# Kernel optimization log

Hardware: AMD Instinct MI355X
Metric: run time of the kernel (lower is better)

Reference implementation:

```python
import jax, jax.numpy as jnp
import numpy as np

N = 20000      # nodes
E = 640000     # edges (avg degree 32)
IN = 32        # input_dim
HID = 256      # hidden_dim
H = 8          # num_heads
Dh = HID // H  # head_dim = 32
TD = 32        # time_dim
L = 3          # num_layers
OUT = 2


def setup_inputs() -> dict:
    key = jax.random.key(0)
    ks = jax.random.split(key, 20)
    def w(k, sh):
        return (jax.random.normal(k, sh, jnp.float32) * 0.05)
    return {
        "x": jax.random.normal(ks[0], (N, IN), jnp.float32),
        "timestamps": jax.random.uniform(ks[1], (N,), jnp.float32),
        "edge_index": jax.random.randint(ks[2], (2, E), 0, N, jnp.int32),
        "batch": jnp.zeros((N,), jnp.int32),
        "time_freq": jax.random.normal(ks[3], (TD // 2,), jnp.float32),
        "inW": w(ks[4], (IN, HID)), "inb": jnp.zeros((HID,), jnp.float32),
        "qW": w(ks[5], (L, HID + TD, HID)), "qb": jnp.zeros((L, HID), jnp.float32),
        "kW": w(ks[6], (L, HID + TD, HID)), "kb": jnp.zeros((L, HID), jnp.float32),
        "vW": w(ks[7], (L, HID, HID)), "vb": jnp.zeros((L, HID), jnp.float32),
        "oW": w(ks[8], (L, HID, HID)), "ob": jnp.zeros((L, HID), jnp.float32),
        "c1W": w(ks[9], (HID, HID // 2)), "c1b": jnp.zeros((HID // 2,), jnp.float32),
        "c2W": w(ks[10], (HID // 2, OUT)), "c2b": jnp.zeros((OUT,), jnp.float32),
    }


def reference(x, timestamps, time_freq, inW, inb, qW, qb, kW, kb, vW, vb,
              oW, ob, c1W, c1b, c2W, c2b, edge_index, batch):
    n = x.shape[0]
    src, dst = edge_index[0], edge_index[1]

    # Functional time encoding (node-level timestamps branch)
    t = (timestamps - timestamps.min()) / (timestamps.max() - timestamps.min() + 1e-8)
    wt = t[:, None] * time_freq[None, :]                      # [N, TD/2]
    tf = jnp.concatenate([jnp.cos(wt), jnp.sin(wt)], axis=-1)  # [N, TD]

    h = x @ inW + inb                                          # [N, HID]
    scale = 1.0 / np.sqrt(Dh).astype(np.float32)

    for l in range(L):
        xt = jnp.concatenate([h, tf], axis=-1)                 # [N, HID+TD]
        Q = (xt @ qW[l] + qb[l]).reshape(n, H, Dh)
        K = (xt @ kW[l] + kb[l]).reshape(n, H, Dh)
        V = (h @ vW[l] + vb[l]).reshape(n, H, Dh)

        # per-edge attention scores [E, H]
        scores = jnp.einsum('ehd,ehd->eh', Q[dst], K[src]) * scale

        # segment softmax over incoming edges of each dst node
        m = jax.ops.segment_max(scores, dst, num_segments=n)   # [N, H]
        e = jnp.exp(scores - m[dst])
        s = jax.ops.segment_sum(e, dst, num_segments=n)        # [N, H]
        att = e / s[dst]                                       # [E, H]

        msgs = att[..., None] * V[src]                         # [E, H, Dh]
        out = jax.ops.segment_sum(msgs, dst, num_segments=n)   # [N, H, Dh]
        out = out.reshape(n, HID) @ oW[l] + ob[l]
        h = jax.nn.elu(out)

    # global mean pool (single graph: batch all zeros)
    cnt = jax.ops.segment_sum(jnp.ones((n, 1), h.dtype), batch, num_segments=1)
    g = jax.ops.segment_sum(h, batch, num_segments=1) / jnp.maximum(cnt, 1.0)

    logits = jax.nn.relu(g @ c1W + c1b) @ c2W + c2b            # [1, OUT]
    return logits
```

## Files before the change

kernel.cpp:

```cpp
#include <hip/hip_runtime.h>
#include <math.h>

#define HID 256
#define TD 32
#define NL 3
#define C1DIM 128
#define OUTDIM 2
#define QKVW 768

using half8  = __attribute__((ext_vector_type(8))) _Float16;
using half4v = __attribute__((ext_vector_type(4))) _Float16;
using half2v = __attribute__((ext_vector_type(2))) _Float16;
using f32x4  = __attribute__((ext_vector_type(4))) float;

typedef __attribute__((address_space(1))) void gbl_void_t;
typedef __attribute__((address_space(3))) void lds_void_t;

__device__ __forceinline__ void load16_to_lds(const void* g, void* l) {
  __builtin_amdgcn_global_load_lds((const gbl_void_t*)g, (lds_void_t*)l, 16, 0, 0);
}

__device__ __forceinline__ float dot8h(half8 a, half8 b, float acc) {
#if __has_builtin(__builtin_amdgcn_fdot2)
  union { half8 v; half2v h2[4]; } ua, ub;
  ua.v = a; ub.v = b;
#pragma unroll
  for (int j = 0; j < 4; ++j) acc = __builtin_amdgcn_fdot2(ua.h2[j], ub.h2[j], acc, false);
  return acc;
#else
#pragma unroll
  for (int j = 0; j < 8; ++j) acc += (float)a[j] * (float)b[j];
  return acc;
#endif
}

__global__ __launch_bounds__(1024) void k_tsmm(const float* __restrict__ ts,
                                               float* __restrict__ mmf,
                                               int* __restrict__ deg, int n) {
  int t = threadIdx.x;
  float lmin = INFINITY, lmax = -INFINITY;
  for (int i = t; i < n; i += 1024) {
    float v = ts[i];
    lmin = fminf(lmin, v);
    lmax = fmaxf(lmax, v);
    deg[i] = 0;
  }
#pragma unroll
  for (int off = 32; off >= 1; off >>= 1) {
    lmin = fminf(lmin, __shfl_xor(lmin, off));
    lmax = fmaxf(lmax, __shfl_xor(lmax, off));
  }
  __shared__ float wmin[16], wmax[16];
  int lane = t & 63, w = t >> 6;
  if (lane == 0) { wmin[w] = lmin; wmax[w] = lmax; }
  __syncthreads();
  if (t == 0) {
    float a = INFINITY, b = -INFINITY;
    for (int i = 0; i < 16; ++i) { a = fminf(a, wmin[i]); b = fmaxf(b, wmax[i]); }
    mmf[0] = a; mmf[1] = b;
  }
}

__global__ void k_enc(const float* __restrict__ ts, const float* __restrict__ freq,
                      const float* __restrict__ mmf, const float* __restrict__ x,
                      _Float16* __restrict__ tfh, _Float16* __restrict__ xh, int n) {
  int idx = blockIdx.x * blockDim.x + threadIdx.x;
  int nt = n * TD;
  if (idx < nt) {
    int node = idx >> 5, j = idx & 31;
    float t = (ts[node] - mmf[0]) / (mmf[1] - mmf[0] + 1e-8f);
    float w = t * freq[j & 15];
    tfh[idx] = (_Float16)((j < 16) ? cosf(w) : sinf(w));
  } else if (idx < nt + n * 32) {
    int i2 = idx - nt;
    xh[i2] = (_Float16)x[i2];
  }
}

__global__ void k_prep(const float* __restrict__ inW, const float* __restrict__ qW,
                       const float* __restrict__ kW, const float* __restrict__ vW,
                       const float* __restrict__ oW, const float* __restrict__ qb,
                       const float* __restrict__ kb, const float* __restrict__ vb,
                       _Float16* __restrict__ inWt, _Float16* __restrict__ qkvWt,
                       float* __restrict__ qkvb, _Float16* __restrict__ oWt) {
  int idx = blockIdx.x * blockDim.x + threadIdx.x;
  const int S0 = 32 * HID;
  const int KQ = HID + TD;
  const int S1 = NL * QKVW * KQ;
  const int S2 = NL * QKVW;
  const int S3 = NL * HID * HID;
  if (idx < S0) {
    int nrow = idx / 32, k = idx - nrow * 32;
    inWt[idx] = (_Float16)inW[k * HID + nrow];
  } else if ((idx -= S0) < S1) {
    int l = idx / (QKVW * KQ);
    int rem = idx - l * (QKVW * KQ);
    int nrow = rem / KQ;
    int k = rem - nrow * KQ;
    float v;
    if (nrow < 256)      v = qW[(size_t)l * KQ * HID + (size_t)k * HID + nrow];
    else if (nrow < 512) v = kW[(size_t)l * KQ * HID + (size_t)k * HID + (nrow - 256)];
    else                 v = (k < HID) ? vW[(size_t)l * HID * HID + (size_t)k * HID + (nrow - 512)] : 0.f;
    qkvWt[idx] = (_Float16)v;
  } else if ((idx -= S1) < S2) {
    int l = idx / QKVW;
    int j = idx - l * QKVW;
    float v;
    if (j < 256)      v = qb[l * HID + j];
    else if (j < 512) v = kb[l * HID + (j - 256)];
    else              v = vb[l * HID + (j - 512)];
    qkvb[idx] = v;
  } else if ((idx -= S2) < S3) {
    int l = idx / (HID * HID);
    int rem = idx - l * (HID * HID);
    int nrow = rem / HID;
    int k = rem - nrow * HID;
    oWt[idx] = (_Float16)oW[(size_t)l * HID * HID + (size_t)k * HID + nrow];
  }
}

__global__ void k_count(const int* __restrict__ dst, int* deg, int e) {
  int i = blockIdx.x * blockDim.x + threadIdx.x;
  if (i < e) atomicAdd(&deg[dst[i]], 1);
}

__global__ __launch_bounds__(256) void k_scan_part(const int* __restrict__ deg,
                                                   int* __restrict__ bsum, int n) {
  int t = threadIdx.x;
  int idx = blockIdx.x * 256 + t;
  int v = (idx < n) ? deg[idx] : 0;
  int lane = t & 63, w = t >> 6;
  int x = v;
#pragma unroll
  for (int off = 1; off < 64; off <<= 1) {
    int y = __shfl_up(x, off);
    if (lane >= off) x += y;
  }
  __shared__ int ws[4];
  if (lane == 63) ws[w] = x;
  __syncthreads();
  if (t == 0) bsum[blockIdx.x] = ws[0] + ws[1] + ws[2] + ws[3];
}

__global__ __launch_bounds__(64) void k_scan_mid(const int* __restrict__ bsum,
                                                 int* __restrict__ boff, int nb) {
  int lane = threadIdx.x;
  int carry = 0;
  for (int base = 0; base < nb; base += 64) {
    int i = base + lane;
    int v = (i < nb) ? bsum[i] : 0;
    int x = v;
#pragma unroll
    for (int off = 1; off < 64; off <<= 1) {
      int y = __shfl_up(x, off);
      if (lane >= off) x += y;
    }
    if (i < nb) boff[i] = carry + x - v;
    carry += __shfl(x, 63);
  }
}

__global__ __launch_bounds__(256) void k_scan_apply(const int* __restrict__ deg,
                                                    const int* __restrict__ boff,
                                                    int* __restrict__ row_ptr,
                                                    int* __restrict__ cursor, int n, int e) {
  int t = threadIdx.x;
  int idx = blockIdx.x * 256 + t;
  int v = (idx < n) ? deg[idx] : 0;
  int lane = t & 63, w = t >> 6;
  int x = v;
#pragma unroll
  for (int off = 1; off < 64; off <<= 1) {
    int y = __shfl_up(x, off);
    if (lane >= off) x += y;
  }
  __shared__ int ws[4];
  if (lane == 63) ws[w] = x;
  __syncthreads();
  int wpre = 0;
  for (int i = 0; i < w; ++i) wpre += ws[i];
  if (idx < n) {
    row_ptr[idx] = boff[blockIdx.x] + wpre + x - v;
    cursor[idx] = 0;
  }
  if (idx == 0) row_ptr[n] = e;
}

__global__ void k_scatter(const int* __restrict__ src, const int* __restrict__ dst,
                          const int* __restrict__ row_ptr, int* cursor,
                          int* __restrict__ colbuf, int e) {
  int i = blockIdx.x * blockDim.x + threadIdx.x;
  if (i >= e) return;
  int d = dst[i];
  int p = atomicAdd(&cursor[d], 1);
  colbuf[row_ptr[d] + p] = src[i];
}

__global__ __launch_bounds__(256) void k_gemm_f16(
    const _Float16* __restrict__ A1, int K1,
    const _Float16* __restrict__ A2, int K2,
    const _Float16* __restrict__ Bt,
    const float* __restrict__ bias,
    _Float16* __restrict__ C,
    _Float16* __restrict__ Qb,
    _Float16* __restrict__ KV,
    int M, int Ncols, int Ktot, int mode) {
  __shared__ half8 smem8[2 * 768];
  char* smem = (char*)smem8;
  const int tid = threadIdx.x;
  const int lane = tid & 63, wave = tid >> 6;
  const int wm = wave >> 1, wn = wave & 1;
  const int row0 = blockIdx.y * 128;
  const int col0 = blockIdx.x * 64;

  auto stage = [&](int buf, int k0) {
    char* sA = smem + buf * 12288;
    char* sB = sA + 8192;
#pragma unroll
    for (int i = 0; i < 2; ++i) {
      int kg = i * 2 + (wave >> 1);
      int row = (wave & 1) * 64 + lane;
      int grow = row0 + row; if (grow > M - 1) grow = M - 1;
      int k = k0 + kg * 8;
      const _Float16* src = (k < K1) ? (A1 + (size_t)grow * K1 + k)
                                     : (A2 + (size_t)grow * K2 + (k - K1));
      load16_to_lds(src, sA + (i * 256 + wave * 64) * 16);
    }
    {
      const _Float16* src = Bt + (size_t)(col0 + lane) * Ktot + k0 + wave * 8;
      load16_to_lds(src, sB + wave * 64 * 16);
    }
  };

  f32x4 acc[4][2];
#pragma unroll
  for (int mf = 0; mf < 4; ++mf)
#pragma unroll
    for (int nf = 0; nf < 2; ++nf) acc[mf][nf] = f32x4{0.f, 0.f, 0.f, 0.f};

  const int nsteps = Ktot >> 5;
  int cur = 0;
  stage(0, 0);
  __syncthreads();
  for (int st = 0; st < nsteps; ++st) {
    if (st + 1 < nsteps) stage(cur ^ 1, (st + 1) * 32);
    char* sA = smem + cur * 12288;
    char* sB = sA + 8192;
    half8 af[4], bf[2];
#pragma unroll
    for (int mf = 0; mf < 4; ++mf) {
      int slot = (lane >> 4) * 128 + wm * 64 + mf * 16 + (lane & 15);
      af[mf] = *(const half8*)(sA + slot * 16);
    }
#pragma unroll
    for (int nf = 0; nf < 2; ++nf) {
      int slot = (lane >> 4) * 64 + wn * 32 + nf * 16 + (lane & 15);
      bf[nf] = *(const half8*)(sB + slot * 16);
    }
#pragma unroll
    for (int mf = 0; mf < 4; ++mf)
#pragma unroll
      for (int nf = 0; nf < 2; ++nf)
        acc[mf][nf] = __builtin_amdgcn_mfma_f32_16x16x32_f16(af[mf], bf[nf], acc[mf][nf], 0, 0, 0);
    __syncthreads();
    cur ^= 1;
  }

  const int rbase = row0 + wm * 64 + (lane >> 4) * 4;
  const int cbase = col0 + wn * 32 + (lane & 15);
#pragma unroll
  for (int nf = 0; nf < 2; ++nf) {
    int col = cbase + nf * 16;
    float bv = bias[col];
    if (mode != 2) {
#pragma unroll
      for (int mf = 0; mf < 4; ++mf) {
#pragma unroll
        for (int r = 0; r < 4; ++r) {
          int row = rbase + mf * 16 + r;
          if (row < M) {
            float v = acc[mf][nf][r] + bv;
            if (mode == 1) v = (v > 0.f) ? v : expm1f(v);
            C[(size_t)row * Ncols + col] = (_Float16)v;
          }
        }
      }
    } else {
      bool isQ = col < 256;
      int cc = col - 256;
      int isV = cc >> 8;
      int c2 = cc & 255;
      int hh = c2 >> 5, dim = c2 & 31;
      size_t kvoff = ((size_t)hh * M) * 64 + isV * 32 + dim;
#pragma unroll
      for (int mf = 0; mf < 4; ++mf) {
#pragma unroll
        for (int r = 0; r < 4; ++r) {
          int row = rbase + mf * 16 + r;
          if (row < M) {
            float v = acc[mf][nf][r] + bv;
            if (isQ) Qb[(size_t)row * HID + col] = (_Float16)v;
            else     KV[kvoff + (size_t)row * 64] = (_Float16)v;
          }
        }
      }
    }
  }
}

__global__ __launch_bounds__(256) void k_attn(const _Float16* __restrict__ Qb,
                                              const _Float16* __restrict__ KV,
                                              const int* __restrict__ row_ptr,
                                              const int* __restrict__ colbuf,
                                              _Float16* __restrict__ out, int n) {
  int h = blockIdx.x & 7;
  int node = (blockIdx.x >> 3) * 64 + (threadIdx.x >> 2);
  if (node >= n) return;
  int j = threadIdx.x & 3;
  const float scale = 0.17677669529663687f;
  const _Float16* KVh = KV + ((size_t)h * n) * 64;

  half8 qh = *(const half8*)(Qb + (size_t)node * HID + h * 32 + j * 8);
  half8 qs;
#pragma unroll
  for (int q = 0; q < 8; ++q) qs[q] = (_Float16)((float)qh[q] * scale);

  int beg = row_ptr[node], end = row_ptr[node + 1];
  float m = -INFINITY, s = 0.f;
  float a[8] = {0.f, 0.f, 0.f, 0.f, 0.f, 0.f, 0.f, 0.f};

  for (int i = beg; i < end; i += 4) {
    half8 kk[4], vv[4];
#pragma unroll
    for (int t = 0; t < 4; ++t) {
      int ii = i + t; if (ii > end - 1) ii = end - 1;
      int sn = colbuf[ii];
      const _Float16* b = KVh + ((size_t)sn) * 64 + j * 8;
      kk[t] = *(const half8*)(b);
      vv[t] = *(const half8*)(b + 32);
    }
    float p[4];
#pragma unroll
    for (int t = 0; t < 4; ++t) p[t] = dot8h(qs, kk[t], 0.f);
#pragma unroll
    for (int t = 0; t < 4; ++t) {
      p[t] += __shfl_xor(p[t], 1);
      p[t] += __shfl_xor(p[t], 2);
      if (i + t >= end) p[t] = -INFINITY;
    }
#pragma unroll
    for (int t = 0; t < 4; ++t) {
      float sc_ = p[t];
      if (sc_ <= m) {
        float e2 = __expf(sc_ - m);
        s += e2;
#pragma unroll
        for (int q = 0; q < 8; ++q) a[q] = fmaf(e2, (float)vv[t][q], a[q]);
      } else {
        float f = __expf(m - sc_);
        s = s * f + 1.f;
#pragma unroll
        for (int q = 0; q < 8; ++q) a[q] = fmaf(a[q], f, (float)vv[t][q]);
        m = sc_;
      }
    }
  }

  float inv = (s > 0.f) ? (1.f / s) : 0.f;
  half8 o;
#pragma unroll
  for (int q = 0; q < 8; ++q) o[q] = (_Float16)(a[q] * inv);
  *(half8*)(out + (size_t)node * HID + h * 32 + j * 8) = o;
}

__global__ __launch_bounds__(256) void k_pool_partial(const _Float16* __restrict__ h,
                                                      float* __restrict__ partial, int n) {
  int b = blockIdx.x, t = threadIdx.x;
  float s = 0.f;
  for (int r = b; r < n; r += 256) s += (float)h[(size_t)r * HID + t];
  partial[b * HID + t] = s;
}

__global__ __launch_bounds__(256) void k_final(const float* __restrict__ partial,
                                               const float* __restrict__ c1W,
                                               const float* __restrict__ c1b,
                                               const float* __restrict__ c2W,
                                               const float* __restrict__ c2b,
                                               float* __restrict__ out, int n) {
  __shared__ float gl[HID];
  __shared__ float r1[C1DIM];
  int t = threadIdx.x;
  float s = 0.f;
  for (int b = 0; b < 256; b++) s += partial[b * HID + t];
  gl[t] = s / (float)n;
  __syncthreads();
  if (t < C1DIM) {
    float a = c1b[t];
    for (int k = 0; k < HID; k++) a += gl[k] * c1W[k * C1DIM + t];
    r1[t] = fmaxf(a, 0.f);
  }
  __syncthreads();
  if (t < OUTDIM) {
    float a = c2b[t];
    for (int k = 0; k < C1DIM; k++) a += r1[k] * c2W[k * OUTDIM + t];
    out[t] = a;
  }
}

extern "C" void kernel_launch(void* const* d_in, const int* in_sizes, int n_in,
                              void* d_out, int out_size, void* d_ws, size_t ws_size,
                              hipStream_t stream) {
  const float* x    = (const float*)d_in[0];
  const float* ts   = (const float*)d_in[1];
  const int*   ei   = (const int*)d_in[2];
  const float* freq = (const float*)d_in[4];
  const float* inW  = (const float*)d_in[5];
  const float* inb  = (const float*)d_in[6];
  const float* qW   = (const float*)d_in[7];
  const float* qb   = (const float*)d_in[8];
  const float* kW   = (const float*)d_in[9];
  const float* kb   = (const float*)d_in[10];
  const float* vW   = (const float*)d_in[11];
  const float* vb   = (const float*)d_in[12];
  const float* oW   = (const float*)d_in[13];
  const float* ob   = (const float*)d_in[14];
  const float* c1W  = (const float*)d_in[15];
  const float* c1b  = (const float*)d_in[16];
  const float* c2W  = (const float*)d_in[17];
  const float* c2b  = (const float*)d_in[18];

  int n = in_sizes[1];
  int e = in_sizes[2] / 2;
  const int* src = ei;
  const int* dst = ei + e;
  int nb = (n + 255) / 256;

  char* w = (char*)d_ws;
  size_t off = 0;
  auto alloc = [&](size_t bytes) -> char* {
    char* p = w + off;
    off = (off + bytes + 255) & ~(size_t)255;
    return p;
  };
  _Float16* tfh     = (_Float16*)alloc((size_t)n * TD * 2);
  _Float16* xh      = (_Float16*)alloc((size_t)n * 32 * 2);
  _Float16* h       = (_Float16*)alloc((size_t)n * HID * 2);
  _Float16* Qbuf    = (_Float16*)alloc((size_t)n * HID * 2);
  _Float16* KV      = (_Float16*)alloc((size_t)n * 512 * 2);
  _Float16* ao      = (_Float16*)alloc((size_t)n * HID * 2);
  _Float16* inWt    = (_Float16*)alloc((size_t)32 * HID * 2);
  _Float16* qkvWt   = (_Float16*)alloc((size_t)NL * QKVW * (HID + TD) * 2);
  float*    qkvb    = (float*)alloc((size_t)NL * QKVW * 4);
  _Float16* oWt     = (_Float16*)alloc((size_t)NL * HID * HID * 2);
  int*      deg     = (int*)alloc((size_t)n * 4);
  int*      cursor  = (int*)alloc((size_t)n * 4);
  int*      row_ptr = (int*)alloc((size_t)(n + 1) * 4);
  int*      colbuf  = (int*)alloc((size_t)e * 4);
  int*      bsum    = (int*)alloc((size_t)nb * 4);
  int*      boff    = (int*)alloc((size_t)nb * 4);
  float*    partial = (float*)alloc((size_t)256 * HID * 4);
  float*    mmf     = (float*)alloc(256);

  int b256 = 256;
  hipLaunchKernelGGL(k_tsmm, dim3(1), dim3(1024), 0, stream, ts, mmf, deg, n);
  hipLaunchKernelGGL(k_enc, dim3((n * 64 + 255) / 256), dim3(b256), 0, stream,
                     ts, freq, mmf, x, tfh, xh, n);
  {
    int total = 32 * HID + NL * QKVW * (HID + TD) + NL * QKVW + NL * HID * HID;
    hipLaunchKernelGGL(k_prep, dim3((total + 255) / 256), dim3(b256), 0, stream,
                       inW, qW, kW, vW, oW, qb, kb, vb, inWt, qkvWt, qkvb, oWt);
  }
  hipLaunchKernelGGL(k_count, dim3((e + 255) / 256), dim3(b256), 0, stream, dst, deg, e);
  hipLaunchKernelGGL(k_scan_part, dim3(nb), dim3(b256), 0, stream, deg, bsum, n);
  hipLaunchKernelGGL(k_scan_mid, dim3(1), dim3(64), 0, stream, bsum, boff, nb);
  hipLaunchKernelGGL(k_scan_apply, dim3(nb), dim3(b256), 0, stream, deg, boff, row_ptr, cursor, n, e);
  hipLaunchKernelGGL(k_scatter, dim3((e + 255) / 256), dim3(b256), 0, stream, src, dst, row_ptr, cursor, colbuf, e);

  dim3 ggrid_h(HID / 64, (n + 127) / 128);
  dim3 ggrid_qkv(QKVW / 64, (n + 127) / 128);
  hipLaunchKernelGGL(k_gemm_f16, ggrid_h, dim3(b256), 0, stream,
                     xh, 32, xh, 32, inWt, inb, h, (_Float16*)nullptr, (_Float16*)nullptr,
                     n, HID, 32, 0);

  int nchunks = (n + 63) / 64;
  for (int l = 0; l < NL; ++l) {
    const _Float16* qkvWtl = qkvWt + (size_t)l * QKVW * (HID + TD);
    const float*    qkvbl  = qkvb + (size_t)l * QKVW;
    const _Float16* oWtl   = oWt + (size_t)l * HID * HID;
    hipLaunchKernelGGL(k_gemm_f16, ggrid_qkv, dim3(b256), 0, stream,
                       h, HID, tfh, TD, qkvWtl, qkvbl, (_Float16*)nullptr, Qbuf, KV,
                       n, QKVW, HID + TD, 2);
    hipLaunchKernelGGL(k_attn, dim3(nchunks * 8), dim3(b256), 0, stream,
                       Qbuf, KV, row_ptr, colbuf, ao, n);
    hipLaunchKernelGGL(k_gemm_f16, ggrid_h, dim3(b256), 0, stream,
                       ao, HID, ao, HID, oWtl, ob + l * HID, h, (_Float16*)nullptr, (_Float16*)nullptr,
                       n, HID, HID, 1);
  }

  hipLaunchKernelGGL(k_pool_partial, dim3(256), dim3(b256), 0, stream, h, partial, n);
  hipLaunchKernelGGL(k_final, dim3(1), dim3(b256), 0, stream, partial, c1W, c1b, c2W, c2b, (float*)d_out, n);
}
```

Before: 481.1 us.

## Software-pipeline K/V gathers in attention kernel and process two nodes per thread

```diff
diff --git a/kernel.cpp b/kernel.cpp
--- a/kernel.cpp
+++ b/kernel.cpp
@@ -314,63 +314,97 @@
                                               const int* __restrict__ colbuf,
                                               _Float16* __restrict__ out, int n) {
   int h = blockIdx.x & 7;
-  int node = (blockIdx.x >> 3) * 64 + (threadIdx.x >> 2);
-  if (node >= n) return;
+  int base = (blockIdx.x >> 3) * 128 + (threadIdx.x >> 2);
   int j = threadIdx.x & 3;
   const float scale = 0.17677669529663687f;
   const _Float16* KVh = KV + ((size_t)h * n) * 64;
 
-  half8 qh = *(const half8*)(Qb + (size_t)node * HID + h * 32 + j * 8);
-  half8 qs;
-#pragma unroll
-  for (int q = 0; q < 8; ++q) qs[q] = (_Float16)((float)qh[q] * scale);
-
-  int beg = row_ptr[node], end = row_ptr[node + 1];
-  float m = -INFINITY, s = 0.f;
-  float a[8] = {0.f, 0.f, 0.f, 0.f, 0.f, 0.f, 0.f, 0.f};
-
-  for (int i = beg; i < end; i += 4) {
-    half8 kk[4], vv[4];
-#pragma unroll
-    for (int t = 0; t < 4; ++t) {
-      int ii = i + t; if (ii > end - 1) ii = end - 1;
-      int sn = colbuf[ii];
-      const _Float16* b = KVh + ((size_t)sn) * 64 + j * 8;
-      kk[t] = *(const half8*)(b);
-      vv[t] = *(const half8*)(b + 32);
-    }
-    float p[4];
-#pragma unroll
-    for (int t = 0; t < 4; ++t) p[t] = dot8h(qs, kk[t], 0.f);
-#pragma unroll
-    for (int t = 0; t < 4; ++t) {
-      p[t] += __shfl_xor(p[t], 1);
-      p[t] += __shfl_xor(p[t], 2);
-      if (i + t >= end) p[t] = -INFINITY;
-    }
-#pragma unroll
-    for (int t = 0; t < 4; ++t) {
-      float sc_ = p[t];
-      if (sc_ <= m) {
-        float e2 = __expf(sc_ - m);
-        s += e2;
-#pragma unroll
-        for (int q = 0; q < 8; ++q) a[q] = fmaf(e2, (float)vv[t][q], a[q]);
-      } else {
-        float f = __expf(m - sc_);
-        s = s * f + 1.f;
-#pragma unroll
-        for (int q = 0; q < 8; ++q) a[q] = fmaf(a[q], f, (float)vv[t][q]);
-        m = sc_;
+#pragma unroll
+  for (int rep = 0; rep < 2; ++rep) {
+    int node = base + rep * 64;
+    if (node >= n) continue;
+
+    half8 qh = *(const half8*)(Qb + (size_t)node * HID + h * 32 + j * 8);
+    half8 qs;
+#pragma unroll
+    for (int q = 0; q < 8; ++q) qs[q] = (_Float16)((float)qh[q] * scale);
+
+    int beg = row_ptr[node], end = row_ptr[node + 1];
+    float m = -INFINITY, s = 0.f;
+    float a[8] = {0.f, 0.f, 0.f, 0.f, 0.f, 0.f, 0.f, 0.f};
+
+    if (beg < end) {
+      auto loadIdx = [&](int c, int (&sn)[4]) {
+#pragma unroll
+        for (int t = 0; t < 4; ++t) {
+          int ii = c + t; if (ii > end - 1) ii = end - 1;
+          sn[t] = colbuf[ii];
+        }
+      };
+      auto loadKV = [&](const int (&sn)[4], half8 (&kk)[4], half8 (&vv)[4]) {
+#pragma unroll
+        for (int t = 0; t < 4; ++t) {
+          const _Float16* b = KVh + ((size_t)sn[t]) * 64 + j * 8;
+          kk[t] = *(const half8*)b;
+          vv[t] = *(const half8*)(b + 32);
+        }
+      };
+      auto computeChunk = [&](int c, half8 (&kk)[4], half8 (&vv)[4]) {
+        float p[4];
+#pragma unroll
+        for (int t = 0; t < 4; ++t) p[t] = dot8h(qs, kk[t], 0.f);
+#pragma unroll
+        for (int t = 0; t < 4; ++t) {
+          p[t] += __shfl_xor(p[t], 1);
+          p[t] += __shfl_xor(p[t], 2);
+          if (c + t >= end) p[t] = -INFINITY;
+        }
+#pragma unroll
+        for (int t = 0; t < 4; ++t) {
+          float sc_ = p[t];
+          if (sc_ <= m) {
+            float e2 = __expf(sc_ - m);
+            s += e2;
+#pragma unroll
+            for (int q = 0; q < 8; ++q) a[q] = fmaf(e2, (float)vv[t][q], a[q]);
+          } else {
+            float f = __expf(m - sc_);
+            s = s * f + 1.f;
+#pragma unroll
+            for (int q = 0; q < 8; ++q) a[q] = fmaf(a[q], f, (float)vv[t][q]);
+            m = sc_;
+          }
+        }
+      };
+
+      int snX[4], snY[4];
+      half8 kkA[4], vvA[4], kkB[4], vvB[4];
+      {
+        int s0[4];
+        loadIdx(beg, s0);
+        loadKV(s0, kkA, vvA);
+        loadIdx(beg + 4, s0);
+        loadKV(s0, kkB, vvB);
       }
-    }
-  }
-
-  float inv = (s > 0.f) ? (1.f / s) : 0.f;
-  half8 o;
-#pragma unroll
-  for (int q = 0; q < 8; ++q) o[q] = (_Float16)(a[q] * inv);
-  *(half8*)(out + (size_t)node * HID + h * 32 + j * 8) = o;
+      loadIdx(beg + 8, snX);
+      loadIdx(beg + 12, snY);
+
+      for (int c = beg; c < end; c += 8) {
+        computeChunk(c, kkA, vvA);
+        loadKV(snX, kkA, vvA);
+        loadIdx(c + 16, snX);
+        computeChunk(c + 4, kkB, vvB);
+        loadKV(snY, kkB, vvB);
+        loadIdx(c + 20, snY);
+      }
+    }
+
+    float inv = (s > 0.f) ? (1.f / s) : 0.f;
+    half8 o;
+#pragma unroll
+    for (int q = 0; q < 8; ++q) o[q] = (_Float16)(a[q] * inv);
+    *(half8*)(out + (size_t)node * HID + h * 32 + j * 8) = o;
+  }
 }
 
 __global__ __launch_bounds__(256) void k_pool_partial(const _Float16* __restrict__ h,
@@ -482,7 +516,7 @@
                      xh, 32, xh, 32, inWt, inb, h, (_Float16*)nullptr, (_Float16*)nullptr,
                      n, HID, 32, 0);
 
-  int nchunks = (n + 63) / 64;
+  int nchunks = (n + 127) / 128;
   for (int l = 0; l < NL; ++l) {
     const _Float16* qkvWtl = qkvWt + (size_t)l * QKVW * (HID + TD);
     const float*    qkvbl  = qkvb + (size_t)l * QKVW;
```

Measured after the change: 488.9 us. About the same (+1.6%).

## Sort attention nodes by degree and fuse timestamp min/max into encoding kernel

Applied to the files above, without the earlier changes.

```diff
diff --git a/kernel.cpp b/kernel.cpp
--- a/kernel.cpp
+++ b/kernel.cpp
@@ -34,47 +34,43 @@
 #endif
 }
 
-__global__ __launch_bounds__(1024) void k_tsmm(const float* __restrict__ ts,
-                                               float* __restrict__ mmf,
-                                               int* __restrict__ deg, int n) {
-  int t = threadIdx.x;
+__global__ __launch_bounds__(256) void k_enc(const float* __restrict__ ts,
+                                             const float* __restrict__ freq,
+                                             const float* __restrict__ x,
+                                             _Float16* __restrict__ tfh,
+                                             _Float16* __restrict__ xh,
+                                             int* __restrict__ deg, int n) {
   float lmin = INFINITY, lmax = -INFINITY;
-  for (int i = t; i < n; i += 1024) {
+  for (int i = threadIdx.x; i < n; i += 256) {
     float v = ts[i];
-    lmin = fminf(lmin, v);
-    lmax = fmaxf(lmax, v);
-    deg[i] = 0;
+    lmin = fminf(lmin, v); lmax = fmaxf(lmax, v);
   }
 #pragma unroll
   for (int off = 32; off >= 1; off >>= 1) {
     lmin = fminf(lmin, __shfl_xor(lmin, off));
     lmax = fmaxf(lmax, __shfl_xor(lmax, off));
   }
-  __shared__ float wmin[16], wmax[16];
-  int lane = t & 63, w = t >> 6;
+  __shared__ float wmin[4], wmax[4];
+  int lane = threadIdx.x & 63, w = threadIdx.x >> 6;
   if (lane == 0) { wmin[w] = lmin; wmax[w] = lmax; }
   __syncthreads();
-  if (t == 0) {
-    float a = INFINITY, b = -INFINITY;
-    for (int i = 0; i < 16; ++i) { a = fminf(a, wmin[i]); b = fmaxf(b, wmax[i]); }
-    mmf[0] = a; mmf[1] = b;
-  }
-}
-
-__global__ void k_enc(const float* __restrict__ ts, const float* __restrict__ freq,
-                      const float* __restrict__ mmf, const float* __restrict__ x,
-                      _Float16* __restrict__ tfh, _Float16* __restrict__ xh, int n) {
-  int idx = blockIdx.x * blockDim.x + threadIdx.x;
+  float tmin = fminf(fminf(wmin[0], wmin[1]), fminf(wmin[2], wmin[3]));
+  float tmax = fmaxf(fmaxf(wmax[0], wmax[1]), fmaxf(wmax[2], wmax[3]));
+  float inv = 1.f / (tmax - tmin + 1e-8f);
   int nt = n * TD;
-  if (idx < nt) {
-    int node = idx >> 5, j = idx & 31;
-    float t = (ts[node] - mmf[0]) / (mmf[1] - mmf[0] + 1e-8f);
-    float w = t * freq[j & 15];
-    tfh[idx] = (_Float16)((j < 16) ? cosf(w) : sinf(w));
-  } else if (idx < nt + n * 32) {
-    int i2 = idx - nt;
-    xh[i2] = (_Float16)x[i2];
-  }
+  int total = n * 64;
+  for (int idx = blockIdx.x * 256 + threadIdx.x; idx < total; idx += gridDim.x * 256) {
+    if (idx < nt) {
+      int node = idx >> 5, j = idx & 31;
+      float t = (ts[node] - tmin) * inv;
+      float wv = t * freq[j & 15];
+      tfh[idx] = (_Float16)((j < 16) ? cosf(wv) : sinf(wv));
+    } else {
+      int i2 = idx - nt;
+      xh[i2] = (_Float16)x[i2];
+    }
+  }
+  for (int i = blockIdx.x * 256 + threadIdx.x; i < n; i += gridDim.x * 256) deg[i] = 0;
 }
 
 __global__ void k_prep(const float* __restrict__ inW, const float* __restrict__ qW,
@@ -124,6 +120,45 @@
   if (i < e) atomicAdd(&deg[dst[i]], 1);
 }
 
+__global__ __launch_bounds__(256) void k_hist(const int* __restrict__ deg,
+                                              int* __restrict__ hist, int n) {
+  __shared__ int lh[256];
+  lh[threadIdx.x] = 0;
+  __syncthreads();
+  int i = blockIdx.x * 256 + threadIdx.x;
+  if (i < n) atomicAdd(&lh[min(deg[i], 255)], 1);
+  __syncthreads();
+  if (lh[threadIdx.x]) atomicAdd(&hist[threadIdx.x], lh[threadIdx.x]);
+}
+
+__global__ __launch_bounds__(256) void k_hscan(const int* __restrict__ hist,
+                                               int* __restrict__ hoff) {
+  int t = threadIdx.x;
+  int v = hist[t];
+  int lane = t & 63, w = t >> 6;
+  int x = v;
+#pragma unroll
+  for (int off = 1; off < 64; off <<= 1) {
+    int y = __shfl_up(x, off);
+    if (lane >= off) x += y;
+  }
+  __shared__ int ws[4];
+  if (lane == 63) ws[w] = x;
+  __syncthreads();
+  int wpre = 0;
+  for (int i = 0; i < w; ++i) wpre += ws[i];
+  hoff[t] = wpre + x - v;
+}
+
+__global__ __launch_bounds__(256) void k_perm(const int* __restrict__ deg,
+                                              int* hoff, int* __restrict__ perm, int n) {
+  int i = blockIdx.x * 256 + threadIdx.x;
+  if (i >= n) return;
+  int b = min(deg[i], 255);
+  int p = atomicAdd(&hoff[b], 1);
+  perm[p] = i;
+}
+
 __global__ __launch_bounds__(256) void k_scan_part(const int* __restrict__ deg,
                                                    int* __restrict__ bsum, int n) {
   int t = threadIdx.x;
@@ -312,10 +347,12 @@
                                               const _Float16* __restrict__ KV,
                                               const int* __restrict__ row_ptr,
                                               const int* __restrict__ colbuf,
+                                              const int* __restrict__ perm,
                                               _Float16* __restrict__ out, int n) {
   int h = blockIdx.x & 7;
-  int node = (blockIdx.x >> 3) * 64 + (threadIdx.x >> 2);
-  if (node >= n) return;
+  int idx = (blockIdx.x >> 3) * 64 + (threadIdx.x >> 2);
+  if (idx >= n) return;
+  int node = perm[idx];
   int j = threadIdx.x & 3;
   const float scale = 0.17677669529663687f;
   const _Float16* KVh = KV + ((size_t)h * n) * 64;
@@ -458,19 +495,24 @@
   int*      colbuf  = (int*)alloc((size_t)e * 4);
   int*      bsum    = (int*)alloc((size_t)nb * 4);
   int*      boff    = (int*)alloc((size_t)nb * 4);
+  int*      hist    = (int*)alloc(256 * 4);
+  int*      hoff    = (int*)alloc(256 * 4);
+  int*      perm    = (int*)alloc((size_t)n * 4);
   float*    partial = (float*)alloc((size_t)256 * HID * 4);
-  float*    mmf     = (float*)alloc(256);
 
   int b256 = 256;
-  hipLaunchKernelGGL(k_tsmm, dim3(1), dim3(1024), 0, stream, ts, mmf, deg, n);
-  hipLaunchKernelGGL(k_enc, dim3((n * 64 + 255) / 256), dim3(b256), 0, stream,
-                     ts, freq, mmf, x, tfh, xh, n);
+  hipMemsetAsync(hist, 0, 256 * 4, stream);
+  hipLaunchKernelGGL(k_enc, dim3(512), dim3(b256), 0, stream,
+                     ts, freq, x, tfh, xh, deg, n);
   {
     int total = 32 * HID + NL * QKVW * (HID + TD) + NL * QKVW + NL * HID * HID;
     hipLaunchKernelGGL(k_prep, dim3((total + 255) / 256), dim3(b256), 0, stream,
                        inW, qW, kW, vW, oW, qb, kb, vb, inWt, qkvWt, qkvb, oWt);
   }
   hipLaunchKernelGGL(k_count, dim3((e + 255) / 256), dim3(b256), 0, stream, dst, deg, e);
+  hipLaunchKernelGGL(k_hist, dim3(nb), dim3(b256), 0, stream, deg, hist, n);
+  hipLaunchKernelGGL(k_hscan, dim3(1), dim3(b256), 0, stream, hist, hoff);
+  hipLaunchKernelGGL(k_perm, dim3(nb), dim3(b256), 0, stream, deg, hoff, perm, n);
   hipLaunchKernelGGL(k_scan_part, dim3(nb), dim3(b256), 0, stream, deg, bsum, n);
   hipLaunchKernelGGL(k_scan_mid, dim3(1), dim3(64), 0, stream, bsum, boff, nb);
   hipLaunchKernelGGL(k_scan_apply, dim3(nb), dim3(b256), 0, stream, deg, boff, row_ptr, cursor, n, e);
@@ -491,7 +533,7 @@
                        h, HID, tfh, TD, qkvWtl, qkvbl, (_Float16*)nullptr, Qbuf, KV,
                        n, QKVW, HID + TD, 2);
     hipLaunchKernelGGL(k_attn, dim3(nchunks * 8), dim3(b256), 0, stream,
-                       Qbuf, KV, row_ptr, colbuf, ao, n);
+                       Qbuf, KV, row_ptr, colbuf, perm, ao, n);
     hipLaunchKernelGGL(k_gemm_f16, ggrid_h, dim3(b256), 0, stream,
                        ao, HID, ao, HID, oWtl, ob + l * HID, h, (_Float16*)nullptr, (_Float16*)nullptr,
                        n, HID, HID, 1);
```

After: 541.2 us. 12.5% more time.
